# Kernel optimization log

Hardware: AMD Instinct MI355X
Metric: run time of the kernel (lower is better)

## Reference

```python
import jax, jax.numpy as jnp
import numpy as np

B, T, H = 64, 4096, 512


def setup_inputs() -> dict:
    key = jax.random.key(0)
    ks = jax.random.split(key, 6)
    x = jax.random.normal(ks[0], (B, T), dtype=jnp.float32)
    # a ~ U(0.95, 0.999) as in torch init (stable decay)
    a = jax.random.uniform(ks[1], (H,), dtype=jnp.float32, minval=0.95, maxval=0.999)
    b = jax.random.uniform(ks[2], (H,), dtype=jnp.float32, minval=-0.5, maxval=0.5)
    c = jax.random.uniform(ks[3], (H,), dtype=jnp.float32, minval=-0.1, maxval=0.1)
    w = jax.random.uniform(ks[4], (H,), dtype=jnp.float32, minval=-0.5, maxval=0.5)
    e = jax.random.uniform(ks[5], (1,), dtype=jnp.float32, minval=-0.1, maxval=0.1)
    return {"x": x, "a": a, "b": b, "c": c, "w": w, "e": e}


def reference(x, a, b, c, w, e):
    # x: [B, T]; a, b, c, w: [H]; e: [1]
    batch = x.shape[0]
    hidden = a.shape[0]

    def step(h, x_t):
        # h: [B, H]; x_t: [B]
        h = a * h + b * x_t[:, None] + c
        return h, None

    h0 = jnp.zeros((batch, hidden), dtype=x.dtype)
    h, _ = jax.lax.scan(step, h0, x.T)  # scan over T
    z = h @ w + e  # [B]
    return z
```

## Files before the change

### kernel.cpp

```cpp
#include <hip/hip_runtime.h>

#define T_LEN 4096
#define H_LEN 512
#define B_LEN 64
#define TCH   32
#define NCHUNK (T_LEN / TCH)

__global__ __launch_bounds__(256) void fused_kernel(
    const float* __restrict__ x,
    const float* __restrict__ a,
    const float* __restrict__ b,
    const float* __restrict__ c,
    const float* __restrict__ w,
    const float* __restrict__ e,
    float* __restrict__ z)
{
    const int tid = threadIdx.x;
    const int blk = blockIdx.x;

    const int row  = tid >> 2;
    const int q    = tid & 3;
    const float* xp = x + (size_t)row * T_LEN + blk * TCH + q * 8;
    const float4 xv0 = ((const float4*)xp)[0];
    const float4 xv1 = ((const float4*)xp)[1];

    __shared__ float wb[H_LEN];
    __shared__ float l2a[H_LEN];
    __shared__ double kred[4];
    __shared__ float Kp;
    for (int j = tid; j < H_LEN; j += 256) {
        wb[j]  = w[j] * b[j];
        l2a[j] = log2f(a[j]);
    }
    if (tid < 4) {
        const int j = blk * 4 + tid;
        const double aj = (double)a[j];
        double p = aj;
#pragma unroll
        for (int i = 0; i < 12; ++i) p *= p;
        const double geo = (1.0 - p) / (1.0 - aj);
        double s = (double)w[j] * (double)c[j] * geo;
        if (blk == 0 && tid == 0) s += (double)e[0];
        kred[tid] = s;
    }
    __syncthreads();

    const int   tt = tid & 31;
    const int   jg = tid >> 5;
    const float k  = (float)(T_LEN - 1 - (blk * TCH + tt));
    const int   j0 = jg * (H_LEN / 8);
    float s = 0.f;
#pragma unroll 8
    for (int jj = 0; jj < H_LEN / 8; ++jj) {
        const int j = j0 + jj;
        s += wb[j] * exp2f(k * l2a[j]);
    }
    __shared__ float part[8][TCH];
    part[jg][tt] = s;
    __syncthreads();
    __shared__ float gl[TCH];
    if (tid < TCH) {
        float acc = 0.f;
#pragma unroll
        for (int g2 = 0; g2 < 8; ++g2) acc += part[g2][tid];
        gl[tid] = acc;
    }
    if (tid == 64) {
        Kp = (float)(kred[0] + kred[1] + kred[2] + kred[3]);
    }
    __syncthreads();

    const float4 gv0 = ((const float4*)gl)[q * 2];
    const float4 gv1 = ((const float4*)gl)[q * 2 + 1];
    float d = xv0.x * gv0.x + xv0.y * gv0.y + xv0.z * gv0.z + xv0.w * gv0.w
            + xv1.x * gv1.x + xv1.y * gv1.y + xv1.z * gv1.z + xv1.w * gv1.w;
    d += __shfl_xor(d, 1, 64);
    d += __shfl_xor(d, 2, 64);
    if (q == 0) atomicAdd(&z[row], d + Kp);
}

extern "C" void kernel_launch(void* const* d_in, const int* in_sizes, int n_in,
                              void* d_out, int out_size, void* d_ws, size_t ws_size,
                              hipStream_t stream) {
    const float* x = (const float*)d_in[0];
    const float* a = (const float*)d_in[1];
    const float* b = (const float*)d_in[2];
    const float* c = (const float*)d_in[3];
    const float* w = (const float*)d_in[4];
    const float* e = (const float*)d_in[5];
    float* out = (float*)d_out;

    fused_kernel<<<NCHUNK, 256, 0, stream>>>(x, a, b, c, w, e, out);
}
```

Baseline: 66.80 us.

## Split into g-vector kernel and per-row dot kernel to remove atomics

```diff
diff --git a/kernel.cpp b/kernel.cpp
--- a/kernel.cpp
+++ b/kernel.cpp
@@ -6,42 +6,20 @@
 #define TCH   32
 #define NCHUNK (T_LEN / TCH)
 
-__global__ __launch_bounds__(256) void fused_kernel(
-    const float* __restrict__ x,
+__global__ __launch_bounds__(256) void g_kernel(
     const float* __restrict__ a,
     const float* __restrict__ b,
-    const float* __restrict__ c,
     const float* __restrict__ w,
-    const float* __restrict__ e,
-    float* __restrict__ z)
+    float* __restrict__ g)
 {
     const int tid = threadIdx.x;
     const int blk = blockIdx.x;
 
-    const int row  = tid >> 2;
-    const int q    = tid & 3;
-    const float* xp = x + (size_t)row * T_LEN + blk * TCH + q * 8;
-    const float4 xv0 = ((const float4*)xp)[0];
-    const float4 xv1 = ((const float4*)xp)[1];
-
     __shared__ float wb[H_LEN];
     __shared__ float l2a[H_LEN];
-    __shared__ double kred[4];
-    __shared__ float Kp;
     for (int j = tid; j < H_LEN; j += 256) {
         wb[j]  = w[j] * b[j];
         l2a[j] = log2f(a[j]);
-    }
-    if (tid < 4) {
-        const int j = blk * 4 + tid;
-        const double aj = (double)a[j];
-        double p = aj;
-#pragma unroll
-        for (int i = 0; i < 12; ++i) p *= p;
-        const double geo = (1.0 - p) / (1.0 - aj);
-        double s = (double)w[j] * (double)c[j] * geo;
-        if (blk == 0 && tid == 0) s += (double)e[0];
-        kred[tid] = s;
     }
     __syncthreads();
 
@@ -58,25 +36,59 @@
     __shared__ float part[8][TCH];
     part[jg][tt] = s;
     __syncthreads();
-    __shared__ float gl[TCH];
     if (tid < TCH) {
         float acc = 0.f;
 #pragma unroll
         for (int g2 = 0; g2 < 8; ++g2) acc += part[g2][tid];
-        gl[tid] = acc;
+        g[blk * TCH + tid] = acc;
     }
-    if (tid == 64) {
-        Kp = (float)(kred[0] + kred[1] + kred[2] + kred[3]);
+}
+
+__global__ __launch_bounds__(256) void dot_kernel(
+    const float* __restrict__ x,
+    const float* __restrict__ a,
+    const float* __restrict__ c,
+    const float* __restrict__ w,
+    const float* __restrict__ e,
+    const float* __restrict__ g,
+    float* __restrict__ z)
+{
+    const int tid = threadIdx.x;
+    const int row = blockIdx.x;
+    const float* xr = x + (size_t)row * T_LEN;
+
+    float local = 0.f;
+#pragma unroll 4
+    for (int seg = 0; seg < 4; ++seg) {
+        const int idx = seg * 1024 + tid * 4;
+        const float4 xv = *(const float4*)(xr + idx);
+        const float4 gv = *(const float4*)(g + idx);
+        local += xv.x * gv.x + xv.y * gv.y + xv.z * gv.z + xv.w * gv.w;
     }
+
+    double kacc = 0.0;
+#pragma unroll 2
+    for (int jj = 0; jj < 2; ++jj) {
+        const int j = tid + jj * 256;
+        const double aj = (double)a[j];
+        double p = aj;
+#pragma unroll
+        for (int i = 0; i < 12; ++i) p *= p;
+        kacc += (double)w[j] * (double)c[j] * (1.0 - p) / (1.0 - aj);
+    }
+    local += (float)kacc;
+    if (tid == 0) local += e[0];
+
+    local += __shfl_xor(local, 1, 64);
+    local += __shfl_xor(local, 2, 64);
+    local += __shfl_xor(local, 4, 64);
+    local += __shfl_xor(local, 8, 64);
+    local += __shfl_xor(local, 16, 64);
+    local += __shfl_xor(local, 32, 64);
+    __shared__ float wsum[4];
+    if ((tid & 63) == 0) wsum[tid >> 6] = local;
     __syncthreads();
-
-    const float4 gv0 = ((const float4*)gl)[q * 2];
-    const float4 gv1 = ((const float4*)gl)[q * 2 + 1];
-    float d = xv0.x * gv0.x + xv0.y * gv0.y + xv0.z * gv0.z + xv0.w * gv0.w
-            + xv1.x * gv1.x + xv1.y * gv1.y + xv1.z * gv1.z + xv1.w * gv1.w;
-    d += __shfl_xor(d, 1, 64);
-    d += __shfl_xor(d, 2, 64);
-    if (q == 0) atomicAdd(&z[row], d + Kp);
+    if (tid == 0) z[row] = wsum[0] + wsum[1] + wsum[2] + wsum[3];
 }
 
 extern "C" void kernel_launch(void* const* d_in, const int* in_sizes, int n_in,
@@ -89,6 +101,8 @@
     const float* w = (const float*)d_in[4];
     const float* e = (const float*)d_in[5];
     float* out = (float*)d_out;
+    float* g   = (float*)d_ws;
 
-    fused_kernel<<<NCHUNK, 256, 0, stream>>>(x, a, b, c, w, e, out);
+    g_kernel<<<NCHUNK, 256, 0, stream>>>(a, b, w, g);
+    dot_kernel<<<B_LEN, 256, 0, stream>>>(x, a, c, w, e, g, out);
 }
```

Result: no change. 67.05 us (+0.4%).
